# Optimization experiments

Hardware: AMD Instinct MI355X
Metric: run time of the kernel (lower is better)

The kernel has to match this reference:

```python
import jax, jax.numpy as jnp
import numpy as np

N = 100000
E = 1600000
IN_DIM, HID_DIM, OUT_DIM = 128, 64, 64


def setup_inputs() -> dict:
    key = jax.random.key(0)
    ks = jax.random.split(key, 8)
    x = jax.random.normal(ks[0], (N, IN_DIM), dtype=jnp.float32)
    src = jax.random.randint(ks[1], (E,), 0, N, dtype=jnp.int32)
    dst = jax.random.randint(ks[2], (E,), 0, N, dtype=jnp.int32)
    edge_index = jnp.stack([src, dst], axis=0)
    edge_weight = jax.random.uniform(ks[3], (E,), dtype=jnp.float32)
    # GCNConv params: lin weight [out, in] (no bias in lin), separate bias [out]
    W1 = jax.random.normal(ks[4], (HID_DIM, IN_DIM), dtype=jnp.float32) / np.sqrt(IN_DIM)
    b1 = jnp.zeros((HID_DIM,), dtype=jnp.float32)
    W2 = jax.random.normal(ks[5], (OUT_DIM, HID_DIM), dtype=jnp.float32) / np.sqrt(HID_DIM)
    b2 = jnp.zeros((OUT_DIM,), dtype=jnp.float32)
    return {"x": x, "edge_index": edge_index, "edge_weight": edge_weight,
            "W1": W1, "b1": b1, "W2": W2, "b2": b2}


def _gcn_conv(x, src, dst, ew, W, b, n_nodes):
    # PyG GCNConv: add self-loops (weight 1), symmetric normalization,
    # linear transform, scatter-add aggregation at dst, then bias.
    loop = jnp.arange(n_nodes, dtype=src.dtype)
    src_full = jnp.concatenate([src, loop])          # [E+N]
    dst_full = jnp.concatenate([dst, loop])          # [E+N]
    ew_full = jnp.concatenate([ew, jnp.ones((n_nodes,), x.dtype)])
    deg = jax.ops.segment_sum(ew_full, dst_full, num_segments=n_nodes)
    dinv = jnp.where(deg > 0, jax.lax.rsqrt(deg), 0.0)  # deg^{-1/2}, inf -> 0
    norm = dinv[src_full] * ew_full * dinv[dst_full]    # [E+N]
    h = x @ W.T                                          # [N, out]
    msgs = h[src_full] * norm[:, None]                   # gather + scale
    out = jax.ops.segment_sum(msgs, dst_full, num_segments=n_nodes)
    return out + b


def reference(x, edge_index, edge_weight, W1, b1, W2, b2):
    src, dst = edge_index[0], edge_index[1]
    h = _gcn_conv(x, src, dst, edge_weight, W1, b1, N)
    h = jax.nn.relu(h)
    # dropout is identity in eval mode (training=False)
    out = _gcn_conv(h, src, dst, edge_weight, W2, b2, N)
    return out
```

## Files before the change

### kernel.cpp

```cpp
#include <hip/hip_runtime.h>
#include <hip/hip_fp16.h>


constexpr float FXS     = 1048576.0f;
constexpr float FXS_INV = 1.0f / 1048576.0f;
constexpr int   SH      = 8;
constexpr int   CAP     = 5120;
constexpr int   NBMAX   = 512;
constexpr int   PW      = 256;
constexpr int   RPW     = 264;
constexpr int   BINA_BLOCKS = 256;

__device__ void binA_body(int bid, int nblocks,
                          const int* __restrict__ src, const int* __restrict__ dst,
                          const float* __restrict__ ew,
                          int* __restrict__ bktcur, int2* __restrict__ stage,
                          int E) {
    __shared__ int cnt[NBMAX], gbase[NBMAX];
    const int tid = threadIdx.x;
    const int nchunks = (E + 2047) >> 11;
    for (int c = bid; c < nchunks; c += nblocks) {
        const int base = c << 11;
        for (int i = tid; i < NBMAX; i += 256) cnt[i] = 0;
        __syncthreads();
        int bkt[8], rank[8], pck[8];
        float w[8];
        #pragma unroll
        for (int j = 0; j < 8; ++j) {
            int e = base + j * 256 + tid;
            bkt[j] = -1;
            if (e < E) {
                int t = dst[e];
                bkt[j] = t >> SH;
                pck[j] = ((t & 255) << 17) | src[e];
                w[j] = ew[e];
                rank[j] = atomicAdd(&cnt[bkt[j]], 1);
            }
        }
        __syncthreads();
        for (int i = tid; i < NBMAX; i += 256)
            if (cnt[i] > 0) gbase[i] = atomicAdd(&bktcur[i], cnt[i]);
        __syncthreads();
        #pragma unroll
        for (int j = 0; j < 8; ++j)
            if (bkt[j] >= 0) {
                int p = gbase[bkt[j]] + rank[j];
                if (p < CAP)
                    stage[(size_t)bkt[j] * CAP + p] =
                        make_int2(pck[j], __float_as_int(w[j]));
            }
        __syncthreads();
    }
}

template <int K, bool RELU, bool BINIT>
__device__ void gemm_body(int bid, const float* __restrict__ X,
                          const float* __restrict__ W,
                          __half* __restrict__ H, int n,
                          const char* __restrict__ flags,
                          const float* __restrict__ dinv,
                          const float* __restrict__ bias,
                          float* __restrict__ OUT) {
    constexpr int BK = 64, BK4 = 16;
    constexpr int XP = 68, WP = 68;
    __shared__ float Xs[64 * XP];
    __shared__ float Ws[BK * WP];
    const int tid = threadIdx.x;
    const int bn0 = bid * 64;
    const int tx = tid & 15, ty = tid >> 4;
    const int f0 = 4 * tx, nl = 4 * ty;

    float acc[4][4] = {};

    for (int kb = 0; kb < K; kb += BK) {
        #pragma unroll
        for (int it = 0; it < 4; ++it) {
            int idx = tid + it * 256;
            int node = idx >> 4, k4 = idx & 15;
            int g = bn0 + node;
            float4 v = make_float4(0.f, 0.f, 0.f, 0.f);
            if (g < n)
                v = *reinterpret_cast<const float4*>(X + (size_t)g * K + kb + 4 * k4);
            if (RELU) {
                v.x = fmaxf(v.x, 0.f); v.y = fmaxf(v.y, 0.f);
                v.z = fmaxf(v.z, 0.f); v.w = fmaxf(v.w, 0.f);
            }
            *reinterpret_cast<float4*>(&Xs[node * XP + 4 * k4]) = v;
        }
        #pragma unroll
        for (int it = 0; it < 4; ++it) {
            int idx = tid + it * 256;
            int feat = idx >> 4, k4 = idx & 15;
            float4 v = *reinterpret_cast<const float4*>(W + feat * K + kb + 4 * k4);
            Ws[(4 * k4 + 0) * WP + feat] = v.x;
            Ws[(4 * k4 + 1) * WP + feat] = v.y;
            Ws[(4 * k4 + 2) * WP + feat] = v.z;
            Ws[(4 * k4 + 3) * WP + feat] = v.w;
        }
        __syncthreads();

        #pragma unroll 4
        for (int k4 = 0; k4 < BK4; ++k4) {
            float4 xv[4], wv[4];
            #pragma unroll
            for (int i = 0; i < 4; ++i)
                xv[i] = *reinterpret_cast<const float4*>(&Xs[(nl + i) * XP + 4 * k4]);
            #pragma unroll
            for (int c = 0; c < 4; ++c)
                wv[c] = *reinterpret_cast<const float4*>(&Ws[(4 * k4 + c) * WP + f0]);
            #pragma unroll
            for (int i = 0; i < 4; ++i) {
                const float xc[4] = {xv[i].x, xv[i].y, xv[i].z, xv[i].w};
                #pragma unroll
                for (int c = 0; c < 4; ++c) {
                    acc[i][0] = fmaf(xc[c], wv[c].x, acc[i][0]);
                    acc[i][1] = fmaf(xc[c], wv[c].y, acc[i][1]);
                    acc[i][2] = fmaf(xc[c], wv[c].z, acc[i][2]);
                    acc[i][3] = fmaf(xc[c], wv[c].w, acc[i][3]);
                }
            }
        }
        __syncthreads();
    }

    #pragma unroll
    for (int i = 0; i < 4; ++i) {
        int g = bn0 + nl + i;
        if (g < n) {
            union { __half h[4]; uint2 u; } cv;
            cv.h[0] = __float2half_rn(acc[i][0]);
            cv.h[1] = __float2half_rn(acc[i][1]);
            cv.h[2] = __float2half_rn(acc[i][2]);
            cv.h[3] = __float2half_rn(acc[i][3]);
            *reinterpret_cast<uint2*>(H + ((size_t)g << 6) + f0) = cv.u;
            if (BINIT) {
                if (flags[g]) {
                    const float d = dinv[g];
                    const float d2 = d * d;
                    const float4 bs = *reinterpret_cast<const float4*>(bias + f0);
                    *reinterpret_cast<float4*>(OUT + ((size_t)g << 6) + f0) =
                        make_float4(fmaf(acc[i][0], d2, bs.x),
                                    fmaf(acc[i][1], d2, bs.y),
                                    fmaf(acc[i][2], d2, bs.z),
                                    fmaf(acc[i][3], d2, bs.w));
                }
            }
        }
    }
}

__global__ __launch_bounds__(256, 4) void k_fat(const int* __restrict__ ei,
                                                const float* __restrict__ ew,
                                                int* __restrict__ bktcur,
                                                int2* __restrict__ stage,
                                                const float* __restrict__ x,
                                                const float* __restrict__ W1,
                                                __half* __restrict__ h16,
                                                int E, int N) {
    if (blockIdx.x < BINA_BLOCKS)
        binA_body(blockIdx.x, BINA_BLOCKS, ei, ei + E, ew, bktcur, stage, E);
    else
        gemm_body<128, false, false>(blockIdx.x - BINA_BLOCKS, x, W1, h16, N,
                                     nullptr, nullptr, nullptr, nullptr);
}

__global__ __launch_bounds__(256, 4) void k_gemm2(const float* __restrict__ X,
                                                  const float* __restrict__ W,
                                                  __half* __restrict__ H, int n,
                                                  const char* __restrict__ flags,
                                                  const float* __restrict__ dinv,
                                                  const float* __restrict__ bias,
                                                  float* __restrict__ OUT) {
    gemm_body<64, true, true>(blockIdx.x, X, W, H, n, flags, dinv, bias, OUT);
}

__global__ __launch_bounds__(256) void k_hist(
    const int2* __restrict__ stage, const int* __restrict__ bsizes,
    float* __restrict__ dinv, int* __restrict__ rowptr,
    int* __restrict__ winstart, char* __restrict__ flags,
    const __half* __restrict__ h16, const float* __restrict__ b1,
    float* __restrict__ agg1, int N, int E) {
    __shared__ unsigned long long hh[256];
    __shared__ int psum[256];
    const int tid = threadIdx.x, b = blockIdx.x;

    int part = 0;
    for (int i = tid; i < b; i += 256) part += min(bsizes[i], CAP);
    psum[tid] = part;
    __syncthreads();
    for (int off = 128; off > 0; off >>= 1) {
        if (tid < off) psum[tid] += psum[tid + off];
        __syncthreads();
    }
    const int base = psum[0];
    const int len = min(bsizes[b], CAP);
    __syncthreads();

    hh[tid] = 0ull;
    __syncthreads();
    for (int i = tid; i < len; i += 256) {
        int2 en = stage[(size_t)b * CAP + i];
        unsigned long long fx = __float2uint_rn(__int_as_float(en.y) * FXS);
        atomicAdd(&hh[((unsigned)en.x) >> 17], (1ull << 32) | fx);
    }
    __syncthreads();

    const int c = (int)(hh[tid] >> 32);
    psum[tid] = c;
    __syncthreads();
    for (int off = 1; off < 256; off <<= 1) {
        int xv = (tid >= off) ? psum[tid - off] : 0;
        __syncthreads();
        psum[tid] += xv;
        __syncthreads();
    }
    const int rs = base + psum[tid] - c;
    const int g = (b << SH) + tid;
    if (g < N) {
        const float dv =
            rsqrtf(1.0f + (float)(hh[tid] & 0xffffffffull) * FXS_INV);
        dinv[g] = dv;
        rowptr[g] = rs;
        const int re = rs + c;
        for (int w = (rs + PW - 1) / PW; w * PW < re; ++w) winstart[w] = g;
        const bool flagged = (c == 0) || ((rs / PW) != ((re - 1) / PW));
        flags[g] = flagged ? 1 : 0;
        if (flagged) {
            const float d2 = dv * dv;
            const __half2* hp = (const __half2*)(h16 + ((size_t)g << 6));
            const float4* pb = (const float4*)b1;
            float4* pa = (float4*)(agg1 + ((size_t)g << 6));
            #pragma unroll
            for (int j = 0; j < 16; ++j) {
                float2 fA = __half22float2(hp[2 * j]);
                float2 fB = __half22float2(hp[2 * j + 1]);
                float4 bb = pb[j];
                pa[j] = make_float4(fmaf(fA.x, d2, bb.x), fmaf(fA.y, d2, bb.y),
                                    fmaf(fB.x, d2, bb.z), fmaf(fB.y, d2, bb.w));
            }
        }
    }
    if (b == 0 && tid == 0) rowptr[N] = E;
}

__global__ __launch_bounds__(256) void k_sort(const int2* __restrict__ stage,
                                              const int* __restrict__ bsizes,
                                              const int* __restrict__ rowptr,
                                              const float* __restrict__ dinv,
                                              int2* __restrict__ edata, int N) {
    __shared__ int cur[256];
    __shared__ float df[256];
    const int tid = threadIdx.x, b = blockIdx.x;
    const int g = (b << SH) + tid;
    if (g < N) {
        cur[tid] = rowptr[g];
        df[tid] = dinv[g];
    }
    __syncthreads();
    const int len = min(bsizes[b], CAP);
    for (int i = tid; i < len; i += 256) {
        int2 en = stage[(size_t)b * CAP + i];
        int local = ((unsigned)en.x) >> 17;
        int s = en.x & 0x1FFFF;
        float nr = dinv[s] * __int_as_float(en.y) * df[local];
        int pos = atomicAdd(&cur[local], 1);
        edata[pos] = make_int2(s, __float_as_int(nr));
    }
}

__global__ __launch_bounds__(256) void k_pull(const int* __restrict__ rowptr,
                                              const int* __restrict__ winstart,
                                              const int2* __restrict__ edata,
                                              const __half* __restrict__ H,
                                              const float* __restrict__ dinv,
                                              const float* __restrict__ bias,
                                              float* __restrict__ AGG,
                                              int nW, int E, int N) {
    __shared__ int2 eb[4][PW];
    __shared__ int rp[4][RPW];
    const int wv = threadIdx.x >> 6, lane = threadIdx.x & 63;
    const int gq = lane >> 4;
    const int f4 = (lane & 15) * 4;
    const float4 bs = *reinterpret_cast<const float4*>(bias + f4);
    const int wid = blockIdx.x * 4 + wv;
    if (wid >= nW) return;
    const int e0 = wid * PW;
    const int e1 = min(e0 + PW, E);
    #pragma unroll
    for (int j = 0; j < PW / 64; ++j) {
        int e = e0 + j * 64 + lane;
        if (e < E) eb[wv][j * 64 + lane] = edata[e];
    }
    const int n0 = winstart[wid];
    #pragma unroll
    for (int j = 0; j < (RPW + 63) / 64; ++j) {
        int idx = j * 64 + lane;
        if (idx < RPW) {
            int nn = n0 + idx;
            rp[wv][idx] = (nn <= N) ? rowptr[nn] : E;
        }
    }
    int n = n0, e = e0;
    int rs = rp[wv][0];
    while (e < e1) {
        const int re = rp[wv][n - n0 + 1];
        const int seg_end = min(re, e1);
        if (seg_end > e) {
            const uint2 hs = *reinterpret_cast<const uint2*>(
                H + ((size_t)n << 6) + f4);
            const float dv = dinv[n];
            float a0 = 0.f, a1 = 0.f, a2 = 0.f, a3 = 0.f;
            int i = e - e0;
            const int iend = seg_end - e0;
            for (; i + 16 <= iend; i += 16) {
                int2 ed[4];
                uint2 hv[4];
                #pragma unroll
                for (int j = 0; j < 4; ++j) ed[j] = eb[wv][i + 4 * j + gq];
                #pragma unroll
                for (int j = 0; j < 4; ++j)
                    hv[j] = *reinterpret_cast<const uint2*>(
                        H + (((size_t)ed[j].x) << 6) + f4);
                #pragma unroll
                for (int j = 0; j < 4; ++j) {
                    const float nr = __int_as_float(ed[j].y);
                    const __half2* ph = reinterpret_cast<const __half2*>(&hv[j]);
                    float2 p01 = __half22float2(ph[0]);
                    float2 p23 = __half22float2(ph[1]);
                    a0 = fmaf(p01.x, nr, a0);
                    a1 = fmaf(p01.y, nr, a1);
                    a2 = fmaf(p23.x, nr, a2);
                    a3 = fmaf(p23.y, nr, a3);
                }
            }
            for (; i < iend; i += 4) {
                int idx = i + gq;
                int2 ed = eb[wv][min(idx, iend - 1)];
                float nr = (idx < iend) ? __int_as_float(ed.y) : 0.f;
                uint2 hv = *reinterpret_cast<const uint2*>(
                    H + (((size_t)ed.x) << 6) + f4);
                const __half2* ph = reinterpret_cast<const __half2*>(&hv);
                float2 p01 = __half22float2(ph[0]);
                float2 p23 = __half22float2(ph[1]);
                a0 = fmaf(p01.x, nr, a0);
                a1 = fmaf(p01.y, nr, a1);
                a2 = fmaf(p23.x, nr, a2);
                a3 = fmaf(p23.y, nr, a3);
            }
            a0 += __shfl_xor(a0, 16); a0 += __shfl_xor(a0, 32);
            a1 += __shfl_xor(a1, 16); a1 += __shfl_xor(a1, 32);
            a2 += __shfl_xor(a2, 16); a2 += __shfl_xor(a2, 32);
            a3 += __shfl_xor(a3, 16); a3 += __shfl_xor(a3, 32);
            if (lane < 16) {
                float* p = AGG + ((size_t)n << 6) + f4;
                if (rs >= e0 && re <= e1) {
                    const float d2 = dv * dv;
                    const __half2* ph = reinterpret_cast<const __half2*>(&hs);
                    float2 s01 = __half22float2(ph[0]);
                    float2 s23 = __half22float2(ph[1]);
                    *reinterpret_cast<float4*>(p) = make_float4(
                        fmaf(s01.x, d2, bs.x) + a0, fmaf(s01.y, d2, bs.y) + a1,
                        fmaf(s23.x, d2, bs.z) + a2, fmaf(s23.y, d2, bs.w) + a3);
                } else {
                    atomicAdd(p + 0, a0);
                    atomicAdd(p + 1, a1);
                    atomicAdd(p + 2, a2);
                    atomicAdd(p + 3, a3);
                }
            }
        }
        e = seg_end;
        rs = re;
        ++n;
    }
}

extern "C" void kernel_launch(void* const* d_in, const int* in_sizes, int n_in,
                              void* d_out, int out_size, void* d_ws, size_t ws_size,
                              hipStream_t stream) {
    const float* x  = (const float*)d_in[0];
    const int*   ei = (const int*)d_in[1];
    const float* ew = (const float*)d_in[2];
    const float* W1 = (const float*)d_in[3];
    const float* b1 = (const float*)d_in[4];
    const float* W2 = (const float*)d_in[5];
    const float* b2 = (const float*)d_in[6];

    const int N = in_sizes[0] / 128;
    const int E = in_sizes[2];
    const int NB = (N + 255) >> SH;
    const int nW = (E + PW - 1) / PW;

    float* ws = (float*)d_ws;
    size_t o = 0;
    float*  dinv     = ws + o;            o += N;
    int*    rowptr   = (int*)(ws + o);    o += (size_t)N + 1;
    int*    winstart = (int*)(ws + o);    o += nW;
    int*    bktcur   = (int*)(ws + o);    o += NBMAX;
    char*   flags    = (char*)(ws + o);   o += (N + 3) / 4;
    o = (o + 1) & ~(size_t)1;
    int2*   edata    = (int2*)(ws + o);   o += 2 * (size_t)E;
    int2*   stage    = (int2*)(ws + o);   o += 2 * (size_t)NB * CAP;
    __half* h16      = (__half*)(ws + o); o += 32 * (size_t)N;
    float*  agg1     = ws + o;            o += 64 * (size_t)N;
    float*  out      = (float*)d_out;

    dim3 blk(256);
    const int gemm_blocks = (N + 63) / 64;

    hipMemsetAsync(bktcur, 0, NBMAX * sizeof(int), stream);
    k_fat<<<BINA_BLOCKS + gemm_blocks, blk, 0, stream>>>(ei, ew, bktcur, stage,
                                                         x, W1, h16, E, N);
    k_hist<<<NB, blk, 0, stream>>>(stage, bktcur, dinv, rowptr, winstart,
                                   flags, h16, b1, agg1, N, E);
    k_sort<<<NB, blk, 0, stream>>>(stage, bktcur, rowptr, dinv, edata, N);

    const int pull_blocks = (nW + 3) / 4;
    k_pull<<<pull_blocks, blk, 0, stream>>>(rowptr, winstart, edata, h16, dinv,
                                            b1, agg1, nW, E, N);
    k_gemm2<<<gemm_blocks, blk, 0, stream>>>(agg1, W2, h16, N, flags, dinv,
                                             b2, out);
    k_pull<<<pull_blocks, blk, 0, stream>>>(rowptr, winstart, edata, h16, dinv,
                                            b2, out, nW, E, N);
}
```

Before: 226.3 us.

## Use 512-node buckets and bound pull rowptr preload by window span

```diff
diff --git a/kernel.cpp b/kernel.cpp
--- a/kernel.cpp
+++ b/kernel.cpp
@@ -4,9 +4,10 @@
 
 constexpr float FXS     = 1048576.0f;
 constexpr float FXS_INV = 1.0f / 1048576.0f;
-constexpr int   SH      = 8;
-constexpr int   CAP     = 5120;
-constexpr int   NBMAX   = 512;
+constexpr int   SH      = 9;
+constexpr int   NPB     = 1 << SH;
+constexpr int   CAP     = 9216;
+constexpr int   NBMAX   = 256;
 constexpr int   PW      = 256;
 constexpr int   RPW     = 264;
 constexpr int   BINA_BLOCKS = 256;
@@ -21,7 +22,7 @@
     const int nchunks = (E + 2047) >> 11;
     for (int c = bid; c < nchunks; c += nblocks) {
         const int base = c << 11;
-        for (int i = tid; i < NBMAX; i += 256) cnt[i] = 0;
+        cnt[tid] = 0;
         __syncthreads();
         int bkt[8], rank[8], pck[8];
         float w[8];
@@ -32,14 +33,13 @@
             if (e < E) {
                 int t = dst[e];
                 bkt[j] = t >> SH;
-                pck[j] = ((t & 255) << 17) | src[e];
+                pck[j] = ((t & (NPB - 1)) << 17) | src[e];
                 w[j] = ew[e];
                 rank[j] = atomicAdd(&cnt[bkt[j]], 1);
             }
         }
         __syncthreads();
-        for (int i = tid; i < NBMAX; i += 256)
-            if (cnt[i] > 0) gbase[i] = atomicAdd(&bktcur[i], cnt[i]);
+        if (cnt[tid] > 0) gbase[tid] = atomicAdd(&bktcur[tid], cnt[tid]);
         __syncthreads();
         #pragma unroll
         for (int j = 0; j < 8; ++j)
@@ -174,19 +174,50 @@
     gemm_body<64, true, true>(blockIdx.x, X, W, H, n, flags, dinv, bias, OUT);
 }
 
+__device__ __forceinline__ void hist_node(int g, int c, int rs,
+                                          unsigned long long hv, int N,
+                                          float* __restrict__ dinv,
+                                          int* __restrict__ rowptr,
+                                          int* __restrict__ winstart,
+                                          char* __restrict__ flags,
+                                          const __half* __restrict__ h16,
+                                          const float* __restrict__ b1,
+                                          float* __restrict__ agg1) {
+    if (g >= N) return;
+    const float dv = rsqrtf(1.0f + (float)(hv & 0xffffffffull) * FXS_INV);
+    dinv[g] = dv;
+    rowptr[g] = rs;
+    const int re = rs + c;
+    for (int w = (rs + PW - 1) / PW; w * PW < re; ++w) winstart[w] = g;
+    const bool flagged = (c == 0) || ((rs / PW) != ((re - 1) / PW));
+    flags[g] = flagged ? 1 : 0;
+    if (flagged) {
+        const float d2 = dv * dv;
+        const __half2* hp = (const __half2*)(h16 + ((size_t)g << 6));
+        const float4* pb = (const float4*)b1;
+        float4* pa = (float4*)(agg1 + ((size_t)g << 6));
+        #pragma unroll
+        for (int j = 0; j < 16; ++j) {
+            float2 fA = __half22float2(hp[2 * j]);
+            float2 fB = __half22float2(hp[2 * j + 1]);
+            float4 bb = pb[j];
+            pa[j] = make_float4(fmaf(fA.x, d2, bb.x), fmaf(fA.y, d2, bb.y),
+                                fmaf(fB.x, d2, bb.z), fmaf(fB.y, d2, bb.w));
+        }
+    }
+}
+
 __global__ __launch_bounds__(256) void k_hist(
     const int2* __restrict__ stage, const int* __restrict__ bsizes,
     float* __restrict__ dinv, int* __restrict__ rowptr,
     int* __restrict__ winstart, char* __restrict__ flags,
     const __half* __restrict__ h16, const float* __restrict__ b1,
-    float* __restrict__ agg1, int N, int E) {
-    __shared__ unsigned long long hh[256];
+    float* __restrict__ agg1, int N, int E, int nW) {
+    __shared__ unsigned long long hh[NPB];
     __shared__ int psum[256];
     const int tid = threadIdx.x, b = blockIdx.x;
 
-    int part = 0;
-    for (int i = tid; i < b; i += 256) part += min(bsizes[i], CAP);
-    psum[tid] = part;
+    psum[tid] = (tid < b) ? min(bsizes[tid], CAP) : 0;
     __syncthreads();
     for (int off = 128; off > 0; off >>= 1) {
         if (tid < off) psum[tid] += psum[tid + off];
@@ -197,6 +228,7 @@
     __syncthreads();
 
     hh[tid] = 0ull;
+    hh[tid + 256] = 0ull;
     __syncthreads();
     for (int i = tid; i < len; i += 256) {
         int2 en = stage[(size_t)b * CAP + i];
@@ -205,8 +237,10 @@
     }
     __syncthreads();
 
-    const int c = (int)(hh[tid] >> 32);
-    psum[tid] = c;
+    const unsigned long long h0 = hh[2 * tid], h1 = hh[2 * tid + 1];
+    const int c0 = (int)(h0 >> 32), c1 = (int)(h1 >> 32);
+    const int s2 = c0 + c1;
+    psum[tid] = s2;
     __syncthreads();
     for (int off = 1; off < 256; off <<= 1) {
         int xv = (tid >= off) ? psum[tid - off] : 0;
@@ -214,33 +248,12 @@
         psum[tid] += xv;
         __syncthreads();
     }
-    const int rs = base + psum[tid] - c;
-    const int g = (b << SH) + tid;
-    if (g < N) {
-        const float dv =
-            rsqrtf(1.0f + (float)(hh[tid] & 0xffffffffull) * FXS_INV);
-        dinv[g] = dv;
-        rowptr[g] = rs;
-        const int re = rs + c;
-        for (int w = (rs + PW - 1) / PW; w * PW < re; ++w) winstart[w] = g;
-        const bool flagged = (c == 0) || ((rs / PW) != ((re - 1) / PW));
-        flags[g] = flagged ? 1 : 0;
-        if (flagged) {
-            const float d2 = dv * dv;
-            const __half2* hp = (const __half2*)(h16 + ((size_t)g << 6));
-            const float4* pb = (const float4*)b1;
-            float4* pa = (float4*)(agg1 + ((size_t)g << 6));
-            #pragma unroll
-            for (int j = 0; j < 16; ++j) {
-                float2 fA = __half22float2(hp[2 * j]);
-                float2 fB = __half22float2(hp[2 * j + 1]);
-                float4 bb = pb[j];
-                pa[j] = make_float4(fmaf(fA.x, d2, bb.x), fmaf(fA.y, d2, bb.y),
-                                    fmaf(fB.x, d2, bb.z), fmaf(fB.y, d2, bb.w));
-            }
-        }
-    }
-    if (b == 0 && tid == 0) rowptr[N] = E;
+    int run = base + psum[tid] - s2;
+    const int g0 = (b << SH) + 2 * tid;
+    hist_node(g0, c0, run, h0, N, dinv, rowptr, winstart, flags, h16, b1, agg1);
+    run += c0;
+    hist_node(g0 + 1, c1, run, h1, N, dinv, rowptr, winstart, flags, h16, b1, agg1);
+    if (b == 0 && tid == 0) { rowptr[N] = E; winstart[nW] = N; }
 }
 
 __global__ __launch_bounds__(256) void k_sort(const int2* __restrict__ stage,
@@ -248,13 +261,17 @@
                                               const int* __restrict__ rowptr,
                                               const float* __restrict__ dinv,
                                               int2* __restrict__ edata, int N) {
-    __shared__ int cur[256];
-    __shared__ float df[256];
+    __shared__ int cur[NPB];
+    __shared__ float df[NPB];
     const int tid = threadIdx.x, b = blockIdx.x;
-    const int g = (b << SH) + tid;
-    if (g < N) {
-        cur[tid] = rowptr[g];
-        df[tid] = dinv[g];
+    #pragma unroll
+    for (int j = 0; j < 2; ++j) {
+        int l = tid + j * 256;
+        int g = (b << SH) + l;
+        if (g < N) {
+            cur[l] = rowptr[g];
+            df[l] = dinv[g];
+        }
     }
     __syncthreads();
     const int len = min(bsizes[b], CAP);
@@ -292,10 +309,10 @@
         if (e < E) eb[wv][j * 64 + lane] = edata[e];
     }
     const int n0 = winstart[wid];
-    #pragma unroll
-    for (int j = 0; j < (RPW + 63) / 64; ++j) {
+    const int spanS = min(winstart[wid + 1] - n0 + 2, RPW);
+    for (int j = 0; j * 64 < spanS; ++j) {
         int idx = j * 64 + lane;
-        if (idx < RPW) {
+        if (idx < spanS) {
             int nn = n0 + idx;
             rp[wv][idx] = (nn <= N) ? rowptr[nn] : E;
         }
@@ -303,7 +320,8 @@
     int n = n0, e = e0;
     int rs = rp[wv][0];
     while (e < e1) {
-        const int re = rp[wv][n - n0 + 1];
+        const int ni = n - n0 + 1;
+        const int re = (ni < spanS) ? rp[wv][ni] : rowptr[n + 1];
         const int seg_end = min(re, e1);
         if (seg_end > e) {
             const uint2 hs = *reinterpret_cast<const uint2*>(
@@ -388,14 +406,14 @@
 
     const int N = in_sizes[0] / 128;
     const int E = in_sizes[2];
-    const int NB = (N + 255) >> SH;
+    const int NB = (N + NPB - 1) >> SH;
     const int nW = (E + PW - 1) / PW;
 
     float* ws = (float*)d_ws;
     size_t o = 0;
     float*  dinv     = ws + o;            o += N;
     int*    rowptr   = (int*)(ws + o);    o += (size_t)N + 1;
-    int*    winstart = (int*)(ws + o);    o += nW;
+    int*    winstart = (int*)(ws + o);    o += (size_t)nW + 1;
     int*    bktcur   = (int*)(ws + o);    o += NBMAX;
     char*   flags    = (char*)(ws + o);   o += (N + 3) / 4;
     o = (o + 1) & ~(size_t)1;
@@ -412,7 +430,7 @@
     k_fat<<<BINA_BLOCKS + gemm_blocks, blk, 0, stream>>>(ei, ew, bktcur, stage,
                                                          x, W1, h16, E, N);
     k_hist<<<NB, blk, 0, stream>>>(stage, bktcur, dinv, rowptr, winstart,
-                                   flags, h16, b1, agg1, N, E);
+                                   flags, h16, b1, agg1, N, E, nW);
     k_sort<<<NB, blk, 0, stream>>>(stage, bktcur, rowptr, dinv, edata, N);
 
     const int pull_blocks = (nW + 3) / 4;
```

Measured after the change: 230.4 us. About the same (+1.8%).

## Store layer-1 aggregate in fp16, trim row-pointer staging, double binning blocks

Applied to the files above, without the earlier changes.

```diff
diff --git a/kernel.cpp b/kernel.cpp
--- a/kernel.cpp
+++ b/kernel.cpp
@@ -5,11 +5,30 @@
 constexpr float FXS     = 1048576.0f;
 constexpr float FXS_INV = 1.0f / 1048576.0f;
 constexpr int   SH      = 8;
+constexpr int   NPB     = 1 << SH;
 constexpr int   CAP     = 5120;
 constexpr int   NBMAX   = 512;
 constexpr int   PW      = 256;
 constexpr int   RPW     = 264;
-constexpr int   BINA_BLOCKS = 256;
+constexpr int   BINA_BLOCKS = 512;
+
+template <typename T> struct is_half16 { static constexpr bool v = false; };
+template <> struct is_half16<__half>  { static constexpr bool v = true; };
+
+__device__ __forceinline__ void atomicAddH2(__half2* addr, float lo, float hi) {
+    unsigned int* ua = reinterpret_cast<unsigned int*>(addr);
+    const __half2 val = __floats2half2_rn(lo, hi);
+    unsigned int old = __atomic_load_n(ua, __ATOMIC_RELAXED);
+    while (true) {
+        __half2 cur;
+        *reinterpret_cast<unsigned int*>(&cur) = old;
+        __half2 sum = __hadd2(cur, val);
+        unsigned int nv = *reinterpret_cast<unsigned int*>(&sum);
+        unsigned int got = atomicCAS(ua, old, nv);
+        if (got == old) break;
+        old = got;
+    }
+}
 
 __device__ void binA_body(int bid, int nblocks,
                           const int* __restrict__ src, const int* __restrict__ dst,
@@ -32,7 +51,7 @@
             if (e < E) {
                 int t = dst[e];
                 bkt[j] = t >> SH;
-                pck[j] = ((t & 255) << 17) | src[e];
+                pck[j] = ((t & (NPB - 1)) << 17) | src[e];
                 w[j] = ew[e];
                 rank[j] = atomicAdd(&cnt[bkt[j]], 1);
             }
@@ -53,8 +72,8 @@
     }
 }
 
-template <int K, bool RELU, bool BINIT>
-__device__ void gemm_body(int bid, const float* __restrict__ X,
+template <int K, bool RELU, bool BINIT, typename TIN>
+__device__ void gemm_body(int bid, const TIN* __restrict__ X,
                           const float* __restrict__ W,
                           __half* __restrict__ H, int n,
                           const char* __restrict__ flags,
@@ -79,8 +98,19 @@
             int node = idx >> 4, k4 = idx & 15;
             int g = bn0 + node;
             float4 v = make_float4(0.f, 0.f, 0.f, 0.f);
-            if (g < n)
-                v = *reinterpret_cast<const float4*>(X + (size_t)g * K + kb + 4 * k4);
+            if (g < n) {
+                if constexpr (is_half16<TIN>::v) {
+                    uint2 raw = *reinterpret_cast<const uint2*>(
+                        X + (size_t)g * K + kb + 4 * k4);
+                    const __half2* ph = reinterpret_cast<const __half2*>(&raw);
+                    float2 fa = __half22float2(ph[0]);
+                    float2 fb = __half22float2(ph[1]);
+                    v = make_float4(fa.x, fa.y, fb.x, fb.y);
+                } else {
+                    v = *reinterpret_cast<const float4*>(
+                        X + (size_t)g * K + kb + 4 * k4);
+                }
+            }
             if (RELU) {
                 v.x = fmaxf(v.x, 0.f); v.y = fmaxf(v.y, 0.f);
                 v.z = fmaxf(v.z, 0.f); v.w = fmaxf(v.w, 0.f);
@@ -160,18 +190,20 @@
     if (blockIdx.x < BINA_BLOCKS)
         binA_body(blockIdx.x, BINA_BLOCKS, ei, ei + E, ew, bktcur, stage, E);
     else
-        gemm_body<128, false, false>(blockIdx.x - BINA_BLOCKS, x, W1, h16, N,
-                                     nullptr, nullptr, nullptr, nullptr);
-}
-
-__global__ __launch_bounds__(256, 4) void k_gemm2(const float* __restrict__ X,
+        gemm_body<128, false, false, float>(blockIdx.x - BINA_BLOCKS, x, W1,
+                                            h16, N, nullptr, nullptr, nullptr,
+                                            nullptr);
+}
+
+__global__ __launch_bounds__(256, 4) void k_gemm2(const __half* __restrict__ X,
                                                   const float* __restrict__ W,
                                                   __half* __restrict__ H, int n,
                                                   const char* __restrict__ flags,
                                                   const float* __restrict__ dinv,
                                                   const float* __restrict__ bias,
                                                   float* __restrict__ OUT) {
-    gemm_body<64, true, true>(blockIdx.x, X, W, H, n, flags, dinv, bias, OUT);
+    gemm_body<64, true, true, __half>(blockIdx.x, X, W, H, n, flags, dinv,
+                                      bias, OUT);
 }
 
 __global__ __launch_bounds__(256) void k_hist(
@@ -179,8 +211,8 @@
     float* __restrict__ dinv, int* __restrict__ rowptr,
     int* __restrict__ winstart, char* __restrict__ flags,
     const __half* __restrict__ h16, const float* __restrict__ b1,
-    float* __restrict__ agg1, int N, int E) {
-    __shared__ unsigned long long hh[256];
+    __half* __restrict__ agg1, int N, int E, int nW) {
+    __shared__ unsigned long long hh[NPB];
     __shared__ int psum[256];
     const int tid = threadIdx.x, b = blockIdx.x;
 
@@ -229,18 +261,22 @@
             const float d2 = dv * dv;
             const __half2* hp = (const __half2*)(h16 + ((size_t)g << 6));
             const float4* pb = (const float4*)b1;
-            float4* pa = (float4*)(agg1 + ((size_t)g << 6));
+            uint2* pa = (uint2*)(agg1 + ((size_t)g << 6));
             #pragma unroll
             for (int j = 0; j < 16; ++j) {
                 float2 fA = __half22float2(hp[2 * j]);
                 float2 fB = __half22float2(hp[2 * j + 1]);
                 float4 bb = pb[j];
-                pa[j] = make_float4(fmaf(fA.x, d2, bb.x), fmaf(fA.y, d2, bb.y),
-                                    fmaf(fB.x, d2, bb.z), fmaf(fB.y, d2, bb.w));
-            }
-        }
-    }
-    if (b == 0 && tid == 0) rowptr[N] = E;
+                union { __half h[4]; uint2 u; } cv;
+                cv.h[0] = __float2half_rn(fmaf(fA.x, d2, bb.x));
+                cv.h[1] = __float2half_rn(fmaf(fA.y, d2, bb.y));
+                cv.h[2] = __float2half_rn(fmaf(fB.x, d2, bb.z));
+                cv.h[3] = __float2half_rn(fmaf(fB.y, d2, bb.w));
+                pa[j] = cv.u;
+            }
+        }
+    }
+    if (b == 0 && tid == 0) { rowptr[N] = E; winstart[nW] = N; }
 }
 
 __global__ __launch_bounds__(256) void k_sort(const int2* __restrict__ stage,
@@ -248,8 +284,8 @@
                                               const int* __restrict__ rowptr,
                                               const float* __restrict__ dinv,
                                               int2* __restrict__ edata, int N) {
-    __shared__ int cur[256];
-    __shared__ float df[256];
+    __shared__ int cur[NPB];
+    __shared__ float df[NPB];
     const int tid = threadIdx.x, b = blockIdx.x;
     const int g = (b << SH) + tid;
     if (g < N) {
@@ -268,13 +304,14 @@
     }
 }
 
+template <bool HOUT>
 __global__ __launch_bounds__(256) void k_pull(const int* __restrict__ rowptr,
                                               const int* __restrict__ winstart,
                                               const int2* __restrict__ edata,
                                               const __half* __restrict__ H,
                                               const float* __restrict__ dinv,
                                               const float* __restrict__ bias,
-                                              float* __restrict__ AGG,
+                                              void* __restrict__ AGGv,
                                               int nW, int E, int N) {
     __shared__ int2 eb[4][PW];
     __shared__ int rp[4][RPW];
@@ -292,10 +329,10 @@
         if (e < E) eb[wv][j * 64 + lane] = edata[e];
     }
     const int n0 = winstart[wid];
-    #pragma unroll
-    for (int j = 0; j < (RPW + 63) / 64; ++j) {
+    const int spanS = min(winstart[wid + 1] - n0 + 2, RPW);
+    for (int j = 0; j * 64 < spanS; ++j) {
         int idx = j * 64 + lane;
-        if (idx < RPW) {
+        if (idx < spanS) {
             int nn = n0 + idx;
             rp[wv][idx] = (nn <= N) ? rowptr[nn] : E;
         }
@@ -303,7 +340,8 @@
     int n = n0, e = e0;
     int rs = rp[wv][0];
     while (e < e1) {
-        const int re = rp[wv][n - n0 + 1];
+        const int ni = n - n0 + 1;
+        const int re = (ni < spanS) ? rp[wv][ni] : rowptr[n + 1];
         const int seg_end = min(re, e1);
         if (seg_end > e) {
             const uint2 hs = *reinterpret_cast<const uint2*>(
@@ -352,20 +390,41 @@
             a2 += __shfl_xor(a2, 16); a2 += __shfl_xor(a2, 32);
             a3 += __shfl_xor(a3, 16); a3 += __shfl_xor(a3, 32);
             if (lane < 16) {
-                float* p = AGG + ((size_t)n << 6) + f4;
-                if (rs >= e0 && re <= e1) {
+                const bool interior = (rs >= e0 && re <= e1);
+                if (interior) {
                     const float d2 = dv * dv;
                     const __half2* ph = reinterpret_cast<const __half2*>(&hs);
                     float2 s01 = __half22float2(ph[0]);
                     float2 s23 = __half22float2(ph[1]);
-                    *reinterpret_cast<float4*>(p) = make_float4(
-                        fmaf(s01.x, d2, bs.x) + a0, fmaf(s01.y, d2, bs.y) + a1,
-                        fmaf(s23.x, d2, bs.z) + a2, fmaf(s23.y, d2, bs.w) + a3);
+                    const float r0 = fmaf(s01.x, d2, bs.x) + a0;
+                    const float r1 = fmaf(s01.y, d2, bs.y) + a1;
+                    const float r2 = fmaf(s23.x, d2, bs.z) + a2;
+                    const float r3 = fmaf(s23.y, d2, bs.w) + a3;
+                    if constexpr (HOUT) {
+                        __half* p = (__half*)AGGv + ((size_t)n << 6) + f4;
+                        union { __half h[4]; uint2 u; } cv;
+                        cv.h[0] = __float2half_rn(r0);
+                        cv.h[1] = __float2half_rn(r1);
+                        cv.h[2] = __float2half_rn(r2);
+                        cv.h[3] = __float2half_rn(r3);
+                        *reinterpret_cast<uint2*>(p) = cv.u;
+                    } else {
+                        float* p = (float*)AGGv + ((size_t)n << 6) + f4;
+                        *reinterpret_cast<float4*>(p) =
+                            make_float4(r0, r1, r2, r3);
+                    }
                 } else {
-                    atomicAdd(p + 0, a0);
-                    atomicAdd(p + 1, a1);
-                    atomicAdd(p + 2, a2);
-                    atomicAdd(p + 3, a3);
+                    if constexpr (HOUT) {
+                        __half* p = (__half*)AGGv + ((size_t)n << 6) + f4;
+                        atomicAddH2(reinterpret_cast<__half2*>(p), a0, a1);
+                        atomicAddH2(reinterpret_cast<__half2*>(p + 2), a2, a3);
+                    } else {
+                        float* p = (float*)AGGv + ((size_t)n << 6) + f4;
+                        atomicAdd(p + 0, a0);
+                        atomicAdd(p + 1, a1);
+                        atomicAdd(p + 2, a2);
+                        atomicAdd(p + 3, a3);
+                    }
                 }
             }
         }
@@ -388,38 +447,40 @@
 
     const int N = in_sizes[0] / 128;
     const int E = in_sizes[2];
-    const int NB = (N + 255) >> SH;
+    const int NB = (N + NPB - 1) >> SH;
     const int nW = (E + PW - 1) / PW;
 
     float* ws = (float*)d_ws;
     size_t o = 0;
     float*  dinv     = ws + o;            o += N;
     int*    rowptr   = (int*)(ws + o);    o += (size_t)N + 1;
-    int*    winstart = (int*)(ws + o);    o += nW;
+    int*    winstart = (int*)(ws + o);    o += (size_t)nW + 1;
     int*    bktcur   = (int*)(ws + o);    o += NBMAX;
     char*   flags    = (char*)(ws + o);   o += (N + 3) / 4;
     o = (o + 1) & ~(size_t)1;
     int2*   edata    = (int2*)(ws + o);   o += 2 * (size_t)E;
     int2*   stage    = (int2*)(ws + o);   o += 2 * (size_t)NB * CAP;
     __half* h16      = (__half*)(ws + o); o += 32 * (size_t)N;
-    float*  agg1     = ws + o;            o += 64 * (size_t)N;
+    __half* agg1     = (__half*)(ws + o); o += 32 * (size_t)N;
     float*  out      = (float*)d_out;
 
     dim3 blk(256);
     const int gemm_blocks = (N + 63) / 64;
 
-    hipMemsetAsync(bktcur, 0, NBMAX * sizeof(int), stream);
+    (void)hipMemsetAsync(bktcur, 0, NBMAX * sizeof(int), stream);
     k_fat<<<BINA_BLOCKS + gemm_blocks, blk, 0, stream>>>(ei, ew, bktcur, stage,
                                                          x, W1, h16, E, N);
     k_hist<<<NB, blk, 0, stream>>>(stage, bktcur, dinv, rowptr, winstart,
-                                   flags, h16, b1, agg1, N, E);
+                                   flags, h16, b1, agg1, N, E, nW);
     k_sort<<<NB, blk, 0, stream>>>(stage, bktcur, rowptr, dinv, edata, N);
 
     const int pull_blocks = (nW + 3) / 4;
-    k_pull<<<pull_blocks, blk, 0, stream>>>(rowptr, winstart, edata, h16, dinv,
-                                            b1, agg1, nW, E, N);
+    k_pull<true><<<pull_blocks, blk, 0, stream>>>(rowptr, winstart, edata, h16,
+                                                  dinv, b1, (void*)agg1,
+                                                  nW, E, N);
     k_gemm2<<<gemm_blocks, blk, 0, stream>>>(agg1, W2, h16, N, flags, dinv,
                                              b2, out);
-    k_pull<<<pull_blocks, blk, 0, stream>>>(rowptr, winstart, edata, h16, dinv,
-                                            b2, out, nW, E, N);
-}
+    k_pull<false><<<pull_blocks, blk, 0, stream>>>(rowptr, winstart, edata, h16,
+                                                   dinv, b2, (void*)out,
+                                                   nW, E, N);
+}
```

Measured after the change: 232.1 us. 1.03x slower.
